# Kernel optimization log

Measured on AMD Instinct MI355X. Metric: run time of the kernel, lower is better.

## Reference

```python
import jax, jax.numpy as jnp
import numpy as np

B, N, D, E = 2, 50000, 128, 640000


def setup_inputs() -> dict:
    key = jax.random.key(0)
    ks = jax.random.split(key, 7)
    x = jax.random.normal(ks[0], (B, N, D), dtype=jnp.float32)
    edge_index = jax.random.randint(ks[1], (2, E), 0, N)
    edge_attr = jax.random.uniform(ks[2], (E,), dtype=jnp.float32)
    s = 1.0 / np.sqrt(D)
    W1 = jax.random.uniform(ks[3], (D, D), jnp.float32, -s, s)
    b1 = jax.random.uniform(ks[4], (D,), jnp.float32, -s, s)
    W2 = jax.random.uniform(ks[5], (D, D), jnp.float32, -s, s)
    b2 = jax.random.uniform(ks[6], (D,), jnp.float32, -s, s)
    return {"x": x, "edge_index": edge_index, "edge_attr": edge_attr,
            "W1": W1, "b1": b1, "W2": W2, "b2": b2}


def _gcn_layer(x, W, b, row, col, norm, n):
    # x: [B, N, D] -> transform then gather-scale-scatter along edges
    h = jnp.einsum('bnd,df->bnf', x, W)
    msg = h[:, row, :] * norm[None, :, None]          # [B, E2, D]
    agg = jax.vmap(lambda m: jax.ops.segment_sum(m, col, num_segments=n))(msg)
    return agg + b


def reference(x, edge_index, edge_attr, W1, b1, W2, b2):
    n = x.shape[1]
    row, col = edge_index[0], edge_index[1]
    # GCNConv default: add self loops (weight 1), symmetric normalization
    loop = jnp.arange(n)
    row2 = jnp.concatenate([row, loop])
    col2 = jnp.concatenate([col, loop])
    w2 = jnp.concatenate([edge_attr, jnp.ones((n,), edge_attr.dtype)])
    deg = jax.ops.segment_sum(w2, col2, num_segments=n)
    dinv = jnp.where(deg > 0, jax.lax.rsqrt(deg), 0.0)
    norm = dinv[row2] * w2 * dinv[col2]               # [E2]
    # dropout is identity in eval mode
    h = jax.nn.relu(_gcn_layer(x, W1, b1, row2, col2, norm, n))
    h = jax.nn.relu(_gcn_layer(h, W2, b2, row2, col2, norm, n))
    return h
```

## Files before the change

kernel.cpp:

```cpp
#include <hip/hip_runtime.h>

#define NNODES 50000
#define NBATCH 2
#define DIM    128
#define NEDGE  640000
#define M_TOT  (NBATCH*NNODES)
#define NXCD   8
#define NBL_N  196

typedef unsigned short u16;
typedef unsigned int   u32;
typedef unsigned long long u64;

typedef __attribute__((ext_vector_type(8))) short bf16x8;
typedef __attribute__((ext_vector_type(4))) float f32x4;

__device__ __forceinline__ float bf2f(u16 u){ return __uint_as_float(((u32)u)<<16); }
__device__ __forceinline__ u16 f2bf(float f){
    u32 x = __float_as_uint(f);
    x += 0x7fffu + ((x>>16)&1u);
    return (u16)(x>>16);
}

__global__ __launch_bounds__(256) void count_k(const int* __restrict__ ei,
                                               const float* __restrict__ ea,
                                               u64* __restrict__ part,
                                               u32* __restrict__ rankpack){
    u32 xcc = __builtin_amdgcn_s_getreg(6164) & 7u;
    int e = blockIdx.x*256 + threadIdx.x;
    if (e < NEDGE){
        int c = ei[NEDGE + e];
        u64 inc = (((u64)__float2uint_rn(ea[e] * 16777216.0f)) << 32) | 1ull;
        u64 old = __hip_atomic_fetch_add(&part[(size_t)xcc*NNODES + c], inc,
                                         __ATOMIC_RELAXED, __HIP_MEMORY_SCOPE_WORKGROUP);
        rankpack[e] = ((u32)old & 0xffffu) | (xcc << 16);
    }
}

__global__ __launch_bounds__(256) void scan1(const u64* __restrict__ part,
                                             int* __restrict__ cnt,
                                             int* __restrict__ poff,
                                             float* __restrict__ dinv,
                                             int* colstart, int* bsum){
    __shared__ int s[256];
    int tid = threadIdx.x;
    int n = blockIdx.x*256 + tid;
    int v = 0;
    if (n < NNODES){
        int run = 0; u64 fsum = 0;
        #pragma unroll
        for (int p = 0; p < NXCD; ++p){
            u64 pv = part[(size_t)p*NNODES + n];
            poff[p*NNODES + n] = run;
            run  += (int)(pv & 0xffffffffu);
            fsum += (pv >> 32);
        }
        cnt[n] = run;
        v = run;
        float deg = 1.0f + (float)fsum * (1.0f/16777216.0f);
        dinv[n] = rsqrtf(deg);
    }
    s[tid] = v; __syncthreads();
    #pragma unroll
    for (int off = 1; off < 256; off <<= 1){
        int t = (tid >= off) ? s[tid-off] : 0;
        __syncthreads();
        s[tid] += t;
        __syncthreads();
    }
    if (n < NNODES) colstart[n] = s[tid] - v;
    if (tid == 255) bsum[blockIdx.x] = s[255];
}

__global__ __launch_bounds__(256) void fill_k(const int* __restrict__ ei,
                                              const float* __restrict__ ea,
                                              const float* __restrict__ dinv,
                                              const int* __restrict__ colstart,
                                              const int* __restrict__ bsum,
                                              const int* __restrict__ poff,
                                              const u32* __restrict__ rankpack,
                                              int* __restrict__ colstartF,
                                              u32* __restrict__ epk){
    __shared__ int s[256];
    __shared__ int pre[256];
    int tid = threadIdx.x;
    int v = (tid < NBL_N) ? bsum[tid] : 0;
    s[tid] = v; __syncthreads();
    #pragma unroll
    for (int off = 1; off < 256; off <<= 1){
        int t = (tid >= off) ? s[tid-off] : 0;
        __syncthreads();
        s[tid] += t;
        __syncthreads();
    }
    pre[tid] = s[tid] - v;
    __syncthreads();

    int e = blockIdx.x*256 + tid;
    if (e < NEDGE){
        int r = ei[e], c = ei[NEDGE + e];
        u32 rp = rankpack[e];
        int base = colstart[c] + pre[c >> 8];
        colstartF[c] = base;
        int pos = base + poff[(rp >> 16)*NNODES + c] + (int)(rp & 0xffffu);
        float w = dinv[r] * ea[e] * dinv[c];
        epk[pos] = (u32)r | ((u32)f2bf(w) << 16);
    }
}

__global__ __launch_bounds__(256) void transposeW(const float* __restrict__ W1, u16* __restrict__ Wt1,
                                                  const float* __restrict__ W2, u16* __restrict__ Wt2,
                                                  u64* __restrict__ part){
    int i = blockIdx.x*256 + threadIdx.x;
    const float* W = (i < 16384) ? W1 : W2;
    u16* Wt       = (i < 16384) ? Wt1 : Wt2;
    int ii = i & 16383;
    int k = ii >> 7, n = ii & 127;
    Wt[n*DIM + k] = f2bf(W[ii]);
    for (int z = i; z < NXCD*NNODES; z += 32768) part[z] = 0;
}

__device__ __forceinline__ bf16x8 load_frag(const float* A, size_t off){
    const float4* ap = (const float4*)(A + off);
    float4 lo = ap[0], hi = ap[1];
    bf16x8 r;
    r[0] = (short)f2bf(lo.x); r[1] = (short)f2bf(lo.y);
    r[2] = (short)f2bf(lo.z); r[3] = (short)f2bf(lo.w);
    r[4] = (short)f2bf(hi.x); r[5] = (short)f2bf(hi.y);
    r[6] = (short)f2bf(hi.z); r[7] = (short)f2bf(hi.w);
    return r;
}
__device__ __forceinline__ bf16x8 load_frag(const u16* A, size_t off){
    return *(const bf16x8*)(A + off);
}

template <typename AT, bool PERM>
__global__ __launch_bounds__(256) void gemm128(const AT* __restrict__ A,
                                               const u16* __restrict__ Wt,
                                               u16* __restrict__ H, int M){
    __shared__ u16 Wl[128][136];
    int tid = threadIdx.x;
    {
        const uint4* src = (const uint4*)Wt;
        #pragma unroll
        for (int j = 0; j < 8; ++j){
            int g = tid + j*256;
            int n = g >> 4;
            int k = (g & 15) * 8;
            *(uint4*)&Wl[n][k] = src[g];
        }
    }
    __syncthreads();

    int wave = tid >> 6, lane = tid & 63;
    int quad = lane >> 4, r = lane & 15;
    int row0 = blockIdx.x*256 + wave*64;

    f32x4 acc[4][8];
    #pragma unroll
    for (int mt = 0; mt < 4; ++mt)
        #pragma unroll
        for (int nt = 0; nt < 8; ++nt)
            acc[mt][nt] = (f32x4){0.f,0.f,0.f,0.f};

    #pragma unroll
    for (int ks = 0; ks < 4; ++ks){
        bf16x8 af[4];
        #pragma unroll
        for (int mt = 0; mt < 4; ++mt){
            int row = row0 + mt*16 + r;
            if (row < M)
                af[mt] = load_frag(A, (size_t)row*DIM + ks*32 + quad*8);
            else
                af[mt] = (bf16x8){0,0,0,0,0,0,0,0};
        }
        #pragma unroll
        for (int nt = 0; nt < 8; ++nt){
            bf16x8 bfr = *(const bf16x8*)&Wl[nt*16 + r][ks*32 + quad*8];
            #pragma unroll
            for (int mt = 0; mt < 4; ++mt)
                acc[mt][nt] = __builtin_amdgcn_mfma_f32_16x16x32_bf16(af[mt], bfr, acc[mt][nt], 0, 0, 0);
        }
    }

    #pragma unroll
    for (int mt = 0; mt < 4; ++mt){
        #pragma unroll
        for (int reg = 0; reg < 4; ++reg){
            int row = row0 + mt*16 + quad*4 + reg;
            if (row < M){
                size_t hrow;
                if (PERM){
                    int b = (row >= NNODES);
                    int n = row - b*NNODES;
                    hrow = (size_t)(2*n + b);
                } else {
                    hrow = (size_t)row;
                }
                #pragma unroll
                for (int nt = 0; nt < 8; ++nt)
                    H[hrow*DIM + nt*16 + r] = f2bf(acc[mt][nt][reg]);
            }
        }
    }
}

template <bool OUT_F32>
__global__ __launch_bounds__(256) void gather6_k(const u16* __restrict__ Hi,
                                                 const u32* __restrict__ epk,
                                                 const int* __restrict__ colstartF,
                                                 const int* __restrict__ cnt,
                                                 const float* __restrict__ dinv,
                                                 const float* __restrict__ bias,
                                                 void* __restrict__ out){
    int wave = threadIdx.x >> 6, lane = threadIdx.x & 63;
    int n = blockIdx.x*4 + wave;
    if (n >= NNODES) return;
    const char* Hb = (const char*)Hi;

    float a0, a1, a2, a3;
    {
        uint2 sv = *(const uint2*)(Hb + (size_t)n*512 + lane*8);
        float dn = dinv[n], dn2 = dn*dn;
        a0 = dn2*__uint_as_float(sv.x << 16);
        a1 = dn2*__uint_as_float(sv.x & 0xffff0000u);
        a2 = dn2*__uint_as_float(sv.y << 16);
        a3 = dn2*__uint_as_float(sv.y & 0xffff0000u);
    }

    int s = colstartF[n], c = cnt[n];
    for (int base = 0; base < c; base += 64){
        int m = min(64, c - base);
        u32 em = 0;
        if (lane < m) em = epk[s + base + lane];
        for (int j = 0; j < m; j += 8){
            #pragma unroll
            for (int g = 0; g < 8; ++g){
                u32 me = __shfl(em, j + g);
                uint2 v = *(const uint2*)(Hb + (size_t)(me & 0xffffu)*512 + lane*8);
                float w = __uint_as_float(me & 0xffff0000u);
                a0 = fmaf(w, __uint_as_float(v.x << 16), a0);
                a1 = fmaf(w, __uint_as_float(v.x & 0xffff0000u), a1);
                a2 = fmaf(w, __uint_as_float(v.y << 16), a2);
                a3 = fmaf(w, __uint_as_float(v.y & 0xffff0000u), a3);
            }
        }
    }

    int sub = lane & 31, b = lane >> 5;
    float4 bb = ((const float4*)bias)[sub];
    a0 = fmaxf(a0 + bb.x, 0.f);
    a1 = fmaxf(a1 + bb.y, 0.f);
    a2 = fmaxf(a2 + bb.z, 0.f);
    a3 = fmaxf(a3 + bb.w, 0.f);
    if (OUT_F32){
        float* O = (float*)out + ((size_t)b*NNODES + n)*DIM + sub*4;
        *(float4*)O = make_float4(a0, a1, a2, a3);
    } else {
        char* O = (char*)out + (size_t)n*512 + lane*8;
        uint2 pk;
        pk.x = (u32)f2bf(a0) | ((u32)f2bf(a1) << 16);
        pk.y = (u32)f2bf(a2) | ((u32)f2bf(a3) << 16);
        *(uint2*)O = pk;
    }
}

extern "C" void kernel_launch(void* const* d_in, const int* in_sizes, int n_in,
                              void* d_out, int out_size, void* d_ws, size_t ws_size,
                              hipStream_t stream){
    const float* x  = (const float*)d_in[0];
    const int*   ei = (const int*)  d_in[1];
    const float* ea = (const float*)d_in[2];
    const float* W1 = (const float*)d_in[3];
    const float* b1 = (const float*)d_in[4];
    const float* W2 = (const float*)d_in[5];
    const float* b2 = (const float*)d_in[6];

    char* p = (char*)d_ws;
    auto alloc = [&](size_t bytes)->char*{ char* r = p; p += (bytes + 511) & ~(size_t)511; return r; };
    u64*   part     = (u64*)  alloc((size_t)NXCD*NNODES*8);
    u32*   rankpack = (u32*)  alloc((size_t)NEDGE*4);
    int*   poff     = (int*)  alloc((size_t)NXCD*NNODES*4);
    float* dinv     = (float*)alloc(NNODES*4);
    int*   cnt      = (int*)  alloc(NNODES*4);
    int*   colstart = (int*)  alloc(NNODES*4);
    int*   colstartF= (int*)  alloc(NNODES*4);
    int*   bsum     = (int*)  alloc(1024);
    u32*   epk      = (u32*)  alloc((size_t)NEDGE*4);
    u16*   Wt1      = (u16*)  alloc(DIM*DIM*2);
    u16*   Wt2      = (u16*)  alloc(DIM*DIM*2);
    u16*   h        = (u16*)  alloc((size_t)M_TOT*DIM*2);
    u16*   o1       = (u16*)  alloc((size_t)M_TOT*DIM*2);

    const int NBL_E = (NEDGE  + 255)/256;
    const int NTILE = (M_TOT + 255)/256;
    const int NBL_G = (NNODES + 3)/4;

    transposeW<<<128, 256, 0, stream>>>(W1, Wt1, W2, Wt2, part);
    count_k<<<NBL_E, 256, 0, stream>>>(ei, ea, part, rankpack);
    scan1  <<<NBL_N, 256, 0, stream>>>(part, cnt, poff, dinv, colstart, bsum);
    fill_k <<<NBL_E, 256, 0, stream>>>(ei, ea, dinv, colstart, bsum, poff, rankpack, colstartF, epk);

    gemm128<float, true ><<<NTILE, 256, 0, stream>>>(x,  Wt1, h, M_TOT);
    gather6_k<false><<<NBL_G, 256, 0, stream>>>(h,  epk, colstartF, cnt, dinv, b1, o1);
    gemm128<u16,   false><<<NTILE, 256, 0, stream>>>(o1, Wt2, h, M_TOT);
    gather6_k<true ><<<NBL_G, 256, 0, stream>>>(h,  epk, colstartF, cnt, dinv, b2, d_out);
}
```

Before: 282.2 us.

## Stage GEMM output through LDS for coalesced stores, halve tile, add nontemporal hints

The GEMM tile is cut from 256 to 128 rows per block, which doubles the block count and lowers accumulator register pressure. The accumulators are written as bf16 into the reused shared W buffer and then stored to global memory as 16-byte row chunks, replacing the scattered 2-byte stores. Nontemporal load and store hints are added to the streaming accesses across the preprocessing, GEMM and gather kernels to reduce cache pollution. The costs are an extra LDS round-trip with barriers, and possibly worse cache behaviour if nontemporal data such as the output h is reused by the gather step.

Result: slower. 296.3 us (+5.0%).

```diff
diff --git a/kernel.cpp b/kernel.cpp
--- a/kernel.cpp
+++ b/kernel.cpp
@@ -14,6 +14,8 @@
 
 typedef __attribute__((ext_vector_type(8))) short bf16x8;
 typedef __attribute__((ext_vector_type(4))) float f32x4;
+typedef __attribute__((ext_vector_type(2))) u32   u32x2;
+typedef __attribute__((ext_vector_type(4))) u32   u32x4;
 
 __device__ __forceinline__ float bf2f(u16 u){ return __uint_as_float(((u32)u)<<16); }
 __device__ __forceinline__ u16 f2bf(float f){
@@ -29,11 +31,12 @@
     u32 xcc = __builtin_amdgcn_s_getreg(6164) & 7u;
     int e = blockIdx.x*256 + threadIdx.x;
     if (e < NEDGE){
-        int c = ei[NEDGE + e];
-        u64 inc = (((u64)__float2uint_rn(ea[e] * 16777216.0f)) << 32) | 1ull;
+        int c = __builtin_nontemporal_load(ei + NEDGE + e);
+        float w = __builtin_nontemporal_load(ea + e);
+        u64 inc = (((u64)__float2uint_rn(w * 16777216.0f)) << 32) | 1ull;
         u64 old = __hip_atomic_fetch_add(&part[(size_t)xcc*NNODES + c], inc,
                                          __ATOMIC_RELAXED, __HIP_MEMORY_SCOPE_WORKGROUP);
-        rankpack[e] = ((u32)old & 0xffffu) | (xcc << 16);
+        __builtin_nontemporal_store(((u32)old & 0xffffu) | (xcc << 16), rankpack + e);
     }
 }
 
@@ -50,7 +53,7 @@
         int run = 0; u64 fsum = 0;
         #pragma unroll
         for (int p = 0; p < NXCD; ++p){
-            u64 pv = part[(size_t)p*NNODES + n];
+            u64 pv = __builtin_nontemporal_load(part + (size_t)p*NNODES + n);
             poff[p*NNODES + n] = run;
             run  += (int)(pv & 0xffffffffu);
             fsum += (pv >> 32);
@@ -98,13 +101,15 @@
 
     int e = blockIdx.x*256 + tid;
     if (e < NEDGE){
-        int r = ei[e], c = ei[NEDGE + e];
-        u32 rp = rankpack[e];
+        int r = __builtin_nontemporal_load(ei + e);
+        int c = __builtin_nontemporal_load(ei + NEDGE + e);
+        float av = __builtin_nontemporal_load(ea + e);
+        u32 rp = __builtin_nontemporal_load(rankpack + e);
         int base = colstart[c] + pre[c >> 8];
         colstartF[c] = base;
         int pos = base + poff[(rp >> 16)*NNODES + c] + (int)(rp & 0xffffu);
-        float w = dinv[r] * ea[e] * dinv[c];
-        epk[pos] = (u32)r | ((u32)f2bf(w) << 16);
+        float w = dinv[r] * av * dinv[c];
+        __builtin_nontemporal_store((u32)r | ((u32)f2bf(w) << 16), epk + pos);
     }
 }
 
@@ -121,8 +126,9 @@
 }
 
 __device__ __forceinline__ bf16x8 load_frag(const float* A, size_t off){
-    const float4* ap = (const float4*)(A + off);
-    float4 lo = ap[0], hi = ap[1];
+    const f32x4* ap = (const f32x4*)(A + off);
+    f32x4 lo = __builtin_nontemporal_load(ap);
+    f32x4 hi = __builtin_nontemporal_load(ap + 1);
     bf16x8 r;
     r[0] = (short)f2bf(lo.x); r[1] = (short)f2bf(lo.y);
     r[2] = (short)f2bf(lo.z); r[3] = (short)f2bf(lo.w);
@@ -131,7 +137,7 @@
     return r;
 }
 __device__ __forceinline__ bf16x8 load_frag(const u16* A, size_t off){
-    return *(const bf16x8*)(A + off);
+    return __builtin_nontemporal_load((const bf16x8*)(A + off));
 }
 
 template <typename AT, bool PERM>
@@ -154,21 +160,22 @@
 
     int wave = tid >> 6, lane = tid & 63;
     int quad = lane >> 4, r = lane & 15;
-    int row0 = blockIdx.x*256 + wave*64;
-
-    f32x4 acc[4][8];
-    #pragma unroll
-    for (int mt = 0; mt < 4; ++mt)
+    int row0 = blockIdx.x*128;
+    int rbase = row0 + wave*32;
+
+    f32x4 acc[2][8];
+    #pragma unroll
+    for (int mt = 0; mt < 2; ++mt)
         #pragma unroll
         for (int nt = 0; nt < 8; ++nt)
             acc[mt][nt] = (f32x4){0.f,0.f,0.f,0.f};
 
     #pragma unroll
     for (int ks = 0; ks < 4; ++ks){
-        bf16x8 af[4];
-        #pragma unroll
-        for (int mt = 0; mt < 4; ++mt){
-            int row = row0 + mt*16 + r;
+        bf16x8 af[2];
+        #pragma unroll
+        for (int mt = 0; mt < 2; ++mt){
+            int row = rbase + mt*16 + r;
             if (row < M)
                 af[mt] = load_frag(A, (size_t)row*DIM + ks*32 + quad*8);
             else
@@ -178,29 +185,36 @@
         for (int nt = 0; nt < 8; ++nt){
             bf16x8 bfr = *(const bf16x8*)&Wl[nt*16 + r][ks*32 + quad*8];
             #pragma unroll
-            for (int mt = 0; mt < 4; ++mt)
+            for (int mt = 0; mt < 2; ++mt)
                 acc[mt][nt] = __builtin_amdgcn_mfma_f32_16x16x32_bf16(af[mt], bfr, acc[mt][nt], 0, 0, 0);
         }
     }
 
-    #pragma unroll
-    for (int mt = 0; mt < 4; ++mt){
-        #pragma unroll
-        for (int reg = 0; reg < 4; ++reg){
-            int row = row0 + mt*16 + quad*4 + reg;
-            if (row < M){
-                size_t hrow;
-                if (PERM){
-                    int b = (row >= NNODES);
-                    int n = row - b*NNODES;
-                    hrow = (size_t)(2*n + b);
-                } else {
-                    hrow = (size_t)row;
-                }
-                #pragma unroll
-                for (int nt = 0; nt < 8; ++nt)
-                    H[hrow*DIM + nt*16 + r] = f2bf(acc[mt][nt][reg]);
+    __syncthreads();
+    #pragma unroll
+    for (int mt = 0; mt < 2; ++mt)
+        #pragma unroll
+        for (int nt = 0; nt < 8; ++nt)
+            #pragma unroll
+            for (int reg = 0; reg < 4; ++reg)
+                Wl[wave*32 + mt*16 + quad*4 + reg][nt*16 + r] = f2bf(acc[mt][nt][reg]);
+    __syncthreads();
+
+    #pragma unroll
+    for (int j = 0; j < 8; ++j){
+        int g = tid + j*256;
+        int rl = g >> 4, ch = g & 15;
+        int row = row0 + rl;
+        if (row < M){
+            size_t hrow;
+            if (PERM){
+                int b = (row >= NNODES);
+                hrow = (size_t)(2*(row - b*NNODES) + b);
+            } else {
+                hrow = (size_t)row;
             }
+            u32x4 vv = *(const u32x4*)&Wl[rl][ch*8];
+            __builtin_nontemporal_store(vv, (u32x4*)((char*)H + hrow*256 + ch*16));
         }
     }
 }
@@ -232,7 +246,7 @@
     for (int base = 0; base < c; base += 64){
         int m = min(64, c - base);
         u32 em = 0;
-        if (lane < m) em = epk[s + base + lane];
+        if (lane < m) em = __builtin_nontemporal_load(epk + s + base + lane);
         for (int j = 0; j < m; j += 8){
             #pragma unroll
             for (int g = 0; g < 8; ++g){
@@ -255,13 +269,14 @@
     a3 = fmaxf(a3 + bb.w, 0.f);
     if (OUT_F32){
         float* O = (float*)out + ((size_t)b*NNODES + n)*DIM + sub*4;
-        *(float4*)O = make_float4(a0, a1, a2, a3);
+        f32x4 vo = (f32x4){a0, a1, a2, a3};
+        __builtin_nontemporal_store(vo, (f32x4*)O);
     } else {
         char* O = (char*)out + (size_t)n*512 + lane*8;
-        uint2 pk;
+        u32x2 pk;
         pk.x = (u32)f2bf(a0) | ((u32)f2bf(a1) << 16);
         pk.y = (u32)f2bf(a2) | ((u32)f2bf(a3) << 16);
-        *(uint2*)O = pk;
+        __builtin_nontemporal_store(pk, (u32x2*)O);
     }
 }
 
@@ -293,7 +308,7 @@
     u16*   o1       = (u16*)  alloc((size_t)M_TOT*DIM*2);
 
     const int NBL_E = (NEDGE  + 255)/256;
-    const int NTILE = (M_TOT + 255)/256;
+    const int NTILE = (M_TOT + 127)/128;
     const int NBL_G = (NNODES + 3)/4;
 
     transposeW<<<128, 256, 0, stream>>>(W1, Wt1, W2, Wt2, part);
```

## Merge independent preprocessing and first GEMM into shared launches

Applied to the files above, without the earlier changes.

The weight transpose now runs in the same launch as the edge-count kernel, and the part buffer is cleared with a memset instead. The edge-fill/CSR placement kernel is merged with the first-layer GEMM into one launch whose blocks branch on block index, so the GEMM tiles and fill blocks run concurrently. This removes launch gaps and lets the compute-bound GEMM overlap the scattered memory-bound fill. In exchange, shared-memory size is sized for the GEMM on every block, and there is an added memset call.

Measured after the change: 293.3 us. 4.0% more time.

```diff
diff --git a/kernel.cpp b/kernel.cpp
--- a/kernel.cpp
+++ b/kernel.cpp
@@ -7,6 +7,8 @@
 #define M_TOT  (NBATCH*NNODES)
 #define NXCD   8
 #define NBL_N  196
+#define NBL_E  2500
+#define NTILE  391
 
 typedef unsigned short u16;
 typedef unsigned int   u32;
@@ -22,18 +24,28 @@
     return (u16)(x>>16);
 }
 
-__global__ __launch_bounds__(256) void count_k(const int* __restrict__ ei,
+__global__ __launch_bounds__(256) void prep1_k(const int* __restrict__ ei,
                                                const float* __restrict__ ea,
                                                u64* __restrict__ part,
-                                               u32* __restrict__ rankpack){
-    u32 xcc = __builtin_amdgcn_s_getreg(6164) & 7u;
-    int e = blockIdx.x*256 + threadIdx.x;
-    if (e < NEDGE){
+                                               u32* __restrict__ rankpack,
+                                               const float* __restrict__ W1, u16* __restrict__ Wt1,
+                                               const float* __restrict__ W2, u16* __restrict__ Wt2){
+    int bid = blockIdx.x;
+    if (bid < NBL_E){
+        u32 xcc = __builtin_amdgcn_s_getreg(6164) & 7u;
+        int e = bid*256 + threadIdx.x;
         int c = ei[NEDGE + e];
         u64 inc = (((u64)__float2uint_rn(ea[e] * 16777216.0f)) << 32) | 1ull;
         u64 old = __hip_atomic_fetch_add(&part[(size_t)xcc*NNODES + c], inc,
                                          __ATOMIC_RELAXED, __HIP_MEMORY_SCOPE_WORKGROUP);
         rankpack[e] = ((u32)old & 0xffffu) | (xcc << 16);
+    } else {
+        int i = (bid - NBL_E)*256 + threadIdx.x;
+        const float* W = (i < 16384) ? W1 : W2;
+        u16* Wt       = (i < 16384) ? Wt1 : Wt2;
+        int ii = i & 16383;
+        int k = ii >> 7, n = ii & 127;
+        Wt[n*DIM + k] = f2bf(W[ii]);
     }
 }
 
@@ -72,54 +84,6 @@
     if (tid == 255) bsum[blockIdx.x] = s[255];
 }
 
-__global__ __launch_bounds__(256) void fill_k(const int* __restrict__ ei,
-                                              const float* __restrict__ ea,
-                                              const float* __restrict__ dinv,
-                                              const int* __restrict__ colstart,
-                                              const int* __restrict__ bsum,
-                                              const int* __restrict__ poff,
-                                              const u32* __restrict__ rankpack,
-                                              int* __restrict__ colstartF,
-                                              u32* __restrict__ epk){
-    __shared__ int s[256];
-    __shared__ int pre[256];
-    int tid = threadIdx.x;
-    int v = (tid < NBL_N) ? bsum[tid] : 0;
-    s[tid] = v; __syncthreads();
-    #pragma unroll
-    for (int off = 1; off < 256; off <<= 1){
-        int t = (tid >= off) ? s[tid-off] : 0;
-        __syncthreads();
-        s[tid] += t;
-        __syncthreads();
-    }
-    pre[tid] = s[tid] - v;
-    __syncthreads();
-
-    int e = blockIdx.x*256 + tid;
-    if (e < NEDGE){
-        int r = ei[e], c = ei[NEDGE + e];
-        u32 rp = rankpack[e];
-        int base = colstart[c] + pre[c >> 8];
-        colstartF[c] = base;
-        int pos = base + poff[(rp >> 16)*NNODES + c] + (int)(rp & 0xffffu);
-        float w = dinv[r] * ea[e] * dinv[c];
-        epk[pos] = (u32)r | ((u32)f2bf(w) << 16);
-    }
-}
-
-__global__ __launch_bounds__(256) void transposeW(const float* __restrict__ W1, u16* __restrict__ Wt1,
-                                                  const float* __restrict__ W2, u16* __restrict__ Wt2,
-                                                  u64* __restrict__ part){
-    int i = blockIdx.x*256 + threadIdx.x;
-    const float* W = (i < 16384) ? W1 : W2;
-    u16* Wt       = (i < 16384) ? Wt1 : Wt2;
-    int ii = i & 16383;
-    int k = ii >> 7, n = ii & 127;
-    Wt[n*DIM + k] = f2bf(W[ii]);
-    for (int z = i; z < NXCD*NNODES; z += 32768) part[z] = 0;
-}
-
 __device__ __forceinline__ bf16x8 load_frag(const float* A, size_t off){
     const float4* ap = (const float4*)(A + off);
     float4 lo = ap[0], hi = ap[1];
@@ -135,10 +99,10 @@
 }
 
 template <typename AT, bool PERM>
-__global__ __launch_bounds__(256) void gemm128(const AT* __restrict__ A,
-                                               const u16* __restrict__ Wt,
-                                               u16* __restrict__ H, int M){
-    __shared__ u16 Wl[128][136];
+__device__ __forceinline__ void gemm_body(const AT* __restrict__ A,
+                                          const u16* __restrict__ Wt,
+                                          u16* __restrict__ H, int M,
+                                          int tileIdx, u16 (*Wl)[136]){
     int tid = threadIdx.x;
     {
         const uint4* src = (const uint4*)Wt;
@@ -154,7 +118,7 @@
 
     int wave = tid >> 6, lane = tid & 63;
     int quad = lane >> 4, r = lane & 15;
-    int row0 = blockIdx.x*256 + wave*64;
+    int row0 = tileIdx*256 + wave*64;
 
     f32x4 acc[4][8];
     #pragma unroll
@@ -203,6 +167,56 @@
             }
         }
     }
+}
+
+template <typename AT, bool PERM>
+__global__ __launch_bounds__(256) void gemm128(const AT* __restrict__ A,
+                                               const u16* __restrict__ Wt,
+                                               u16* __restrict__ H, int M){
+    __shared__ u16 Wl[128][136];
+    gemm_body<AT, PERM>(A, Wt, H, M, blockIdx.x, Wl);
+}
+
+__global__ __launch_bounds__(256) void fillgemm_k(const int* __restrict__ ei,
+                                                  const float* __restrict__ ea,
+                                                  const float* __restrict__ dinv,
+                                                  const int* __restrict__ colstart,
+                                                  const int* __restrict__ bsum,
+                                                  const int* __restrict__ poff,
+                                                  const u32* __restrict__ rankpack,
+                                                  int* __restrict__ colstartF,
+                                                  u32* __restrict__ epk,
+                                                  const float* __restrict__ x,
+                                                  const u16* __restrict__ Wt1,
+                                                  u16* __restrict__ h){
+    __shared__ u16 Wl[128][136];
+    if (blockIdx.x < NTILE){
+        gemm_body<float, true>(x, Wt1, h, M_TOT, blockIdx.x, Wl);
+        return;
+    }
+    int* s   = (int*)&Wl[0][0];
+    int* pre = s + 256;
+    int tid = threadIdx.x;
+    int v = (tid < NBL_N) ? bsum[tid] : 0;
+    s[tid] = v; __syncthreads();
+    #pragma unroll
+    for (int off = 1; off < 256; off <<= 1){
+        int t = (tid >= off) ? s[tid-off] : 0;
+        __syncthreads();
+        s[tid] += t;
+        __syncthreads();
+    }
+    pre[tid] = s[tid] - v;
+    __syncthreads();
+
+    int e = (blockIdx.x - NTILE)*256 + tid;
+    int r = ei[e], c = ei[NEDGE + e];
+    u32 rp = rankpack[e];
+    int base = colstart[c] + pre[c >> 8];
+    colstartF[c] = base;
+    int pos = base + poff[(rp >> 16)*NNODES + c] + (int)(rp & 0xffffu);
+    float w = dinv[r] * ea[e] * dinv[c];
+    epk[pos] = (u32)r | ((u32)f2bf(w) << 16);
 }
 
 template <bool OUT_F32>
@@ -292,17 +306,14 @@
     u16*   h        = (u16*)  alloc((size_t)M_TOT*DIM*2);
     u16*   o1       = (u16*)  alloc((size_t)M_TOT*DIM*2);
 
-    const int NBL_E = (NEDGE  + 255)/256;
-    const int NTILE = (M_TOT + 255)/256;
     const int NBL_G = (NNODES + 3)/4;
 
-    transposeW<<<128, 256, 0, stream>>>(W1, Wt1, W2, Wt2, part);
-    count_k<<<NBL_E, 256, 0, stream>>>(ei, ea, part, rankpack);
+    hipMemsetAsync(part, 0, (size_t)NXCD*NNODES*8, stream);
+    prep1_k<<<NBL_E + 128, 256, 0, stream>>>(ei, ea, part, rankpack, W1, Wt1, W2, Wt2);
     scan1  <<<NBL_N, 256, 0, stream>>>(part, cnt, poff, dinv, colstart, bsum);
-    fill_k <<<NBL_E, 256, 0, stream>>>(ei, ea, dinv, colstart, bsum, poff, rankpack, colstartF, epk);
-
-    gemm128<float, true ><<<NTILE, 256, 0, stream>>>(x,  Wt1, h, M_TOT);
+    fillgemm_k<<<NTILE + NBL_E, 256, 0, stream>>>(ei, ea, dinv, colstart, bsum, poff,
+                                                  rankpack, colstartF, epk, x, Wt1, h);
     gather6_k<false><<<NBL_G, 256, 0, stream>>>(h,  epk, colstartF, cnt, dinv, b1, o1);
-    gemm128<u16,   false><<<NTILE, 256, 0, stream>>>(o1, Wt2, h, M_TOT);
+    gemm128<u16, false><<<NTILE, 256, 0, stream>>>(o1, Wt2, h, M_TOT);
     gather6_k<true ><<<NBL_G, 256, 0, stream>>>(h,  epk, colstartF, cnt, dinv, b2, d_out);
 }
```
